# Optimization experiments

Measured on AMD Instinct MI355X. Metric: run time of the kernel, lower is better.

## Reference

```python
import jax, jax.numpy as jnp
import numpy as np
import math

B, S, H, E, TOPK, NHEADS = 8, 512, 1024, 8, 2, 8
CAP = int(B * S * 1.5 * TOPK / E)  # 1536


def _linear(x, w, b):
    # torch nn.Linear convention: y = x @ w.T + b, w: [out, in]
    return x @ w.T + b


def _mha(x, in_w, in_b, out_w, out_b, n_heads):
    # torch nn.MultiheadAttention self-attention, eval mode (no dropout)
    Bx, Sx, D = x.shape
    dh = D // n_heads
    qkv = x @ in_w.T + in_b                      # [B,S,3D]
    q, k, v = jnp.split(qkv, 3, axis=-1)
    def heads(t):
        return t.reshape(Bx, Sx, n_heads, dh).transpose(0, 2, 1, 3)  # [B,h,S,dh]
    q, k, v = heads(q), heads(k), heads(v)
    scores = jnp.einsum('bhqd,bhkd->bhqk', q, k) / math.sqrt(dh)
    attn = jax.nn.softmax(scores, axis=-1)
    o = jnp.einsum('bhqk,bhkd->bhqd', attn, v)   # [B,h,S,dh]
    o = o.transpose(0, 2, 1, 3).reshape(Bx, Sx, D)
    return o @ out_w.T + out_b


def setup_inputs() -> dict:
    key = jax.random.key(0)
    ks = jax.random.split(key, 24)
    sc = 0.02
    d = {
        'hidden_states': jax.random.normal(ks[0], (B, S, H), jnp.float32),
        'pos_emb': jax.random.normal(ks[1], (S, H), jnp.float32) * sc,
        'se_w1': jax.random.normal(ks[2], (H // 4, 1), jnp.float32) * sc,
        'se_b1': jnp.zeros((H // 4,), jnp.float32),
        'se_w2': jax.random.normal(ks[3], (H // 4, H // 4), jnp.float32) * sc,
        'se_b2': jnp.zeros((H // 4,), jnp.float32),
        'sexp_w': jax.random.normal(ks[4], (H, H // 4), jnp.float32) * sc,
        'sexp_b': jnp.zeros((H,), jnp.float32),
        'te_w1': jax.random.normal(ks[5], (H, H + 2), jnp.float32) * sc,
        'te_b1': jnp.zeros((H,), jnp.float32),
        'te_w2': jax.random.normal(ks[6], (H, H), jnp.float32) * sc,
        'te_b2': jnp.zeros((H,), jnp.float32),
        'attn_in_w': jax.random.normal(ks[7], (3 * H, H), jnp.float32) * sc,
        'attn_in_b': jnp.zeros((3 * H,), jnp.float32),
        'attn_out_w': jax.random.normal(ks[8], (H, H), jnp.float32) * sc,
        'attn_out_b': jnp.zeros((H,), jnp.float32),
        'tr_w1': jax.random.normal(ks[9], (H, H), jnp.float32) * sc,
        'tr_b1': jnp.zeros((H,), jnp.float32),
        'tr_w2': jax.random.normal(ks[10], (E, H), jnp.float32) * sc,
        'tr_b2': jnp.zeros((E,), jnp.float32),
    }
    return d


def reference(hidden_states, pos_emb, se_w1, se_b1, se_w2, se_b2, sexp_w, sexp_b,
              te_w1, te_b1, te_w2, te_b2, attn_in_w, attn_in_b, attn_out_w, attn_out_b,
              tr_w1, tr_b1, tr_w2, tr_b2):
    b, s, h = hidden_states.shape
    timestamps = jnp.arange(s, dtype=hidden_states.dtype)           # [S]
    seasonality = jnp.sin(timestamps * 2 * jnp.pi / 24)             # [S]
    ts_b = jnp.broadcast_to(timestamps, (b, s))
    se_b = jnp.broadcast_to(seasonality, (b, s))

    position_embeddings = pos_emb[:s][None]                          # [1,S,H]
    seas = jax.nn.relu(_linear(se_b[..., None], se_w1, se_b1))       # [B,S,H/4]
    seas = _linear(seas, se_w2, se_b2)
    seasonal_embeddings = _linear(seas, sexp_w, sexp_b)              # [B,S,H]

    time_features = jnp.stack([ts_b, se_b], axis=-1)                 # [B,S,2]
    combined = jnp.concatenate([hidden_states, time_features], -1)   # [B,S,H+2]
    enc = jax.nn.relu(_linear(combined, te_w1, te_b1))
    enc = _linear(enc, te_w2, te_b2)
    enc = enc + position_embeddings + seasonal_embeddings
    enc = _mha(enc, attn_in_w, attn_in_b, attn_out_w, attn_out_b, NHEADS)

    logits = _linear(jax.nn.relu(_linear(enc, tr_w1, tr_b1)), tr_w2, tr_b2)  # [B,S,E]
    router_probs = jax.nn.softmax(logits, axis=-1)
    top_k_probs, top_k_idx = jax.lax.top_k(router_probs, TOPK)
    top_k_probs = top_k_probs / top_k_probs.sum(-1, keepdims=True)

    capacity = int(b * s * 1.5 * TOPK / E)
    # top-k indices are distinct per token, so summed one-hots replicate the
    # python loop's slot-0 writes exactly.
    onehot = jax.nn.one_hot(top_k_idx, E, dtype=router_probs.dtype)  # [B,S,K,E]
    disp0 = onehot.sum(axis=2)                                        # [B,S,E]
    comb0 = jnp.einsum('bske,bsk->bse', onehot, top_k_probs)          # [B,S,E]
    dispatch = jnp.zeros((b, s, E, capacity), router_probs.dtype).at[:, :, :, 0].set(disp0)
    combine = jnp.zeros((b, s, E, capacity), router_probs.dtype).at[:, :, :, 0].set(comb0)

    p_mean = router_probs.mean(axis=(0, 1))
    aux_loss = jnp.sum(p_mean * jnp.log(p_mean * E + 1e-9))
    return dispatch, combine, router_probs, aux_loss
```

## Files before the change

kernel.cpp:

```cpp
#include <hip/hip_runtime.h>
#include <hip/hip_bf16.h>


#define Hh 1024

typedef __attribute__((ext_vector_type(8))) short short8v;
typedef __attribute__((ext_vector_type(4))) float f32x4;

static __device__ __forceinline__ ushort f2bf(float x) {
  uint u = __float_as_uint(x);
  u += 0x7FFF + ((u >> 16) & 1);
  return (ushort)(u >> 16);
}
static __device__ __forceinline__ float bf2f(ushort h) {
  return __uint_as_float(((uint)h) << 16);
}

#define KBARRIER() do { \
    __builtin_amdgcn_sched_barrier(0); \
    asm volatile("s_waitcnt lgkmcnt(0)" ::: "memory"); \
    __builtin_amdgcn_sched_barrier(0); \
    __builtin_amdgcn_s_barrier(); \
    __builtin_amdgcn_sched_barrier(0); \
  } while (0)

template<int EPI, bool RELU, bool HAS_BN, bool HAS_BSN>
__global__ __launch_bounds__(256, 2) void mgemm_k(
    const ushort* __restrict__ A, int lda, long long sAmaj, long long sAmin, int aHi, int aLo,
    const ushort* __restrict__ Bf, int BNT, int BKC, long long sBmaj, long long sBmin,
    float* __restrict__ Cf, ushort* __restrict__ Ch, int ldc, long long sCmaj, long long sCmin,
    int splitOff,
    ushort* __restrict__ pK, ushort* __restrict__ pV,
    int Kd, int zdiv,
    const float* __restrict__ bN, const float* __restrict__ bSN, int ldbs, int smod,
    float alpha,
    char* __restrict__ zout, long long zbase, long long zlimit)
{
  int gx = gridDim.x, gy = gridDim.y;
  int lin = (blockIdx.z * gy + blockIdx.y) * gx + blockIdx.x;
  int nwg = gx * gy * gridDim.z;
  int cpx = nwg >> 3;
  int swz = (lin & 7) * cpx + (lin >> 3);
  int bz = swz / (gx * gy);
  int rem = swz - bz * (gx * gy);
  int by = rem / gx, bx = rem - by * gx;

  int zj = bz / zdiv, zi = bz - zj * zdiv;
  A += (size_t)zj * sAmaj + (size_t)zi * sAmin;
  const ushort* bfb = Bf + (size_t)zj * sBmaj + (size_t)zi * sBmin;
  long long coff = (long long)zj * sCmaj + (long long)zi * sCmin;

  int m0 = by * 64, n0 = bx * 128;

  __shared__ __align__(16) ushort smem[16384];

  int t = threadIdx.x;
  int l = t & 63, w = t >> 6;
  int wm = w >> 1, wn = w & 1;

  f32x4 acc[2][4];
#pragma unroll
  for (int i = 0; i < 2; ++i)
#pragma unroll
    for (int j = 0; j < 4; ++j) acc[i][j] = (f32x4){0.f, 0.f, 0.f, 0.f};

  int srow = t >> 2;
  int sc = t & 3;
  const ushort* gAh = A + (size_t)(m0 + srow) * lda + aHi + sc * 8;
  const ushort* gAl = A + (size_t)(m0 + srow) * lda + aLo + sc * 8;
  int wo = (srow * 64 + sc * 16) ^ (((srow >> 1) & 7) << 4);

  int aoff[2];
#pragma unroll
  for (int mi = 0; mi < 2; ++mi) {
    int row = wm * 32 + mi * 16 + (l & 15);
    aoff[mi] = (row * 64 + (l >> 4) * 16) ^ (((row >> 1) & 7) << 4);
  }

  const ushort* bph[4];
  const ushort* bpl[4];
  int ntg0 = (n0 >> 4) + wn * 4;
#pragma unroll
  for (int ni = 0; ni < 4; ++ni) {
    bph[ni] = bfb + ((size_t)(ntg0 + ni) * BKC) * 512 + l * 8;
    bpl[ni] = bfb + ((size_t)(BNT + ntg0 + ni) * BKC) * 512 + l * 8;
  }

  int4 a0h, a0l, a1h, a1l;
  short8v B0h[4], B0l[4], B1h[4], B1l[4];

#define LOADA0(s) { a0h = *(const int4*)(gAh + (s)*32); a0l = *(const int4*)(gAl + (s)*32); }
#define LOADA1(s) { a1h = *(const int4*)(gAh + (s)*32); a1l = *(const int4*)(gAl + (s)*32); }
#define STOREA(h, lo2, base) { char* nb = (char*)smem + (base); \
    *(int4*)(nb + wo) = h; *(int4*)(nb + 4096 + wo) = lo2; }
#define LOADB(BH, BL, s) { _Pragma("unroll") \
    for (int ni = 0; ni < 4; ++ni) { \
      BH[ni] = *(const short8v*)(bph[ni] + (size_t)(s) * 512); \
      BL[ni] = *(const short8v*)(bpl[ni] + (size_t)(s) * 512); } }
#define MFMA_STEP(ahb, alb, BH, BL) { \
    short8v ah[2], al[2]; \
    _Pragma("unroll") for (int mi = 0; mi < 2; ++mi) \
      ah[mi] = *(const short8v*)((char*)smem + (ahb) + aoff[mi]); \
    _Pragma("unroll") for (int mi = 0; mi < 2; ++mi) \
      al[mi] = *(const short8v*)((char*)smem + (alb) + aoff[mi]); \
    _Pragma("unroll") for (int ni = 0; ni < 4; ++ni) \
      _Pragma("unroll") for (int mi = 0; mi < 2; ++mi) \
        acc[mi][ni] = __builtin_amdgcn_mfma_f32_16x16x32_bf16(ah[mi], BH[ni], acc[mi][ni], 0, 0, 0); \
    _Pragma("unroll") for (int ni = 0; ni < 4; ++ni) \
      _Pragma("unroll") for (int mi = 0; mi < 2; ++mi) \
        acc[mi][ni] = __builtin_amdgcn_mfma_f32_16x16x32_bf16(al[mi], BH[ni], acc[mi][ni], 0, 0, 0); \
    _Pragma("unroll") for (int ni = 0; ni < 4; ++ni) \
      _Pragma("unroll") for (int mi = 0; mi < 2; ++mi) \
        acc[mi][ni] = __builtin_amdgcn_mfma_f32_16x16x32_bf16(ah[mi], BL[ni], acc[mi][ni], 0, 0, 0); }

  int nt = Kd >> 5;
  LOADA0(0); LOADB(B0h, B0l, 0);
  LOADA1(1); LOADB(B1h, B1l, 1);
  STOREA(a0h, a0l, 0);
  KBARRIER();
  for (int s2 = 0; s2 < nt; s2 += 2) {
    if (s2 + 2 < nt) LOADA0(s2 + 2);
    MFMA_STEP(0, 4096, B0h, B0l);
    if (s2 + 2 < nt) LOADB(B0h, B0l, s2 + 2);
    STOREA(a1h, a1l, 8192);
    KBARRIER();
    if (s2 + 3 < nt) LOADA1(s2 + 3);
    MFMA_STEP(8192, 12288, B1h, B1l);
    if (s2 + 3 < nt) LOADB(B1h, B1l, s2 + 3);
    if (s2 + 2 < nt) STOREA(a0h, a0l, 0);
    KBARRIER();
  }
#undef LOADA0
#undef LOADA1
#undef STOREA
#undef LOADB
#undef MFMA_STEP

#pragma unroll
  for (int mi = 0; mi < 2; ++mi)
#pragma unroll
    for (int j = 0; j < 4; ++j) {
      int m = m0 + wm * 32 + mi * 16 + (l >> 4) * 4 + j;
#pragma unroll
      for (int ni = 0; ni < 4; ++ni) {
        int n = n0 + wn * 64 + ni * 16 + (l & 15);
        float x = acc[mi][ni][j] * alpha;
        if (HAS_BN) x += bN[n];
        if (HAS_BSN) x += bSN[(size_t)(m % smod) * ldbs + n];
        if (RELU) x = fmaxf(x, 0.f);
        acc[mi][ni][j] = x;
      }
    }

  if (EPI == 0) {
    float* Fs = (float*)smem;
#pragma unroll
    for (int mi = 0; mi < 2; ++mi)
#pragma unroll
      for (int j = 0; j < 4; ++j) {
        int r = wm * 32 + mi * 16 + (l >> 4) * 4 + j;
#pragma unroll
        for (int ni = 0; ni < 4; ++ni) {
          int c = wn * 64 + ni * 16 + (l & 15);
          *(float*)((char*)Fs + ((r * 512 + c * 4) ^ ((r & 7) << 4))) = acc[mi][ni][j];
        }
      }
    __syncthreads();
#pragma unroll
    for (int r8 = 0; r8 < 8; ++r8) {
      int idx = r8 * 256 + t;
      int row = idx >> 5, slot = idx & 31;
      int4 v = *(const int4*)((char*)Fs + ((row * 512 + slot * 16) ^ ((row & 7) << 4)));
      *(int4*)(Cf + coff + (size_t)(m0 + row) * ldc + n0 + slot * 4) = v;
    }
  } else {
    ushort* Es = smem;
    bool isQ = (EPI == 1) || (n0 < 1024);
    bool isK = (EPI == 2) && !isQ && (n0 < 2048);
    int bb = m0 >> 9, s0 = m0 & 511;
    int hh2 = isK ? ((n0 - 1024) >> 7) : ((n0 - 2048) >> 7);
    size_t kvb = (size_t)(bb * 8 + hh2) * 131072;
#pragma unroll
    for (int pass = 0; pass < 2; ++pass) {
      if (!(EPI == 2 && !isQ && !isK)) {
#pragma unroll
        for (int mi = 0; mi < 2; ++mi)
#pragma unroll
          for (int j = 0; j < 4; ++j) {
            int lr = wm * 32 + mi * 16 + (l >> 4) * 4 + j;
#pragma unroll
            for (int ni = 0; ni < 4; ++ni) {
              int lcb = (wn * 64 + ni * 16 + (l & 15)) * 2;
              float x = acc[mi][ni][j];
              ushort h = f2bf(x);
              ushort vv = (pass == 0) ? h : f2bf(x - bf2f(h));
              *(ushort*)((char*)Es + ((lr * 256 + lcb) ^ ((lr & 7) << 4))) = vv;
            }
          }
      } else {
#pragma unroll
        for (int mi = 0; mi < 2; ++mi)
#pragma unroll
          for (int j = 0; j < 4; ++j) {
            int cc = (wm * 32 + mi * 16 + (l >> 4) * 4 + j) * 2;
#pragma unroll
            for (int ni = 0; ni < 4; ++ni) {
              int rr = wn * 64 + ni * 16 + (l & 15);
              float x = acc[mi][ni][j];
              ushort h = f2bf(x);
              ushort vv = (pass == 0) ? h : f2bf(x - bf2f(h));
              *(ushort*)((char*)Es + ((rr * 128 + cc) ^ ((rr & 7) << 4))) = vv;
            }
          }
      }
      __syncthreads();
      if (isQ) {
        int off = (pass == 0) ? 0 : splitOff;
#pragma unroll
        for (int r = 0; r < 4; ++r) {
          int idx = r * 256 + t;
          int row = idx >> 4, cb = (idx & 15) * 16;
          int4 v = *(const int4*)((char*)Es + ((row * 256 + cb) ^ ((row & 7) << 4)));
          *(int4*)((char*)(Ch + coff + (size_t)(m0 + row) * ldc + off + n0) + cb) = v;
        }
      } else if (isK) {
#pragma unroll
        for (int sw = 0; sw < 4; ++sw) {
          int idx = sw * 256 + t;
          int f = idx >> 6, l2 = idx & 63;
          int st = f >> 2, dc = f & 3;
          int row = st * 16 + (l2 & 15);
          int colB = (dc * 32 + ((l2 >> 4) << 3)) * 2;
          short8v v = *(const short8v*)((char*)Es + ((row * 256 + colB) ^ ((row & 7) << 4)));
          *(short8v*)(pK + kvb + (size_t)((pass * 32 + (s0 >> 4) + st) * 4 + dc) * 512 + l2 * 8) = v;
        }
      } else {
#pragma unroll
        for (int sw = 0; sw < 4; ++sw) {
          int idx = sw * 256 + t;
          int f = idx >> 6, l2 = idx & 63;
          int dt = f >> 1, sch = f & 1;
          int row = dt * 16 + (l2 & 15);
          int colB = (sch * 32 + ((l2 >> 4) << 3)) * 2;
          short8v v = *(const short8v*)((char*)Es + ((row * 128 + colB) ^ ((row & 7) << 4)));
          *(short8v*)(pV + kvb + (size_t)((pass * 8 + dt) * 16 + (s0 >> 5) + sch) * 512 + l2 * 8) = v;
        }
      }
      if (pass == 0) __syncthreads();
    }
  }

  if (zlimit > 0) {
    long long zo = zbase + (long long)lin * 65536LL;
    if (zo < zlimit) {
      long long n16 = (zlimit - zo) >> 4;
      if (n16 > 4096) n16 = 4096;
      float4* zp = (float4*)(zout + zo);
      float4 zz = make_float4(0.f, 0.f, 0.f, 0.f);
      for (long long i = t; i < n16; i += 256) zp[i] = zz;
    }
  }
}

__global__ __launch_bounds__(64) void convertf_k(
    const float* __restrict__ W, int ldw, ushort* __restrict__ Wf, int NT, int KC)
{
  int kc = blockIdx.x, nt2 = blockIdx.y, l = threadIdx.x;
  const float* src = W + (size_t)(nt2 * 16 + (l & 15)) * ldw + kc * 32 + ((l >> 4) << 3);
  ushort h8[8], l8[8];
#pragma unroll
  for (int j = 0; j < 8; ++j) {
    float x = src[j];
    h8[j] = f2bf(x);
    l8[j] = f2bf(x - bf2f(h8[j]));
  }
  *(int4*)(Wf + ((size_t)nt2 * KC + kc) * 512 + l * 8) = *(int4*)h8;
  *(int4*)(Wf + ((size_t)(NT + nt2) * KC + kc) * 512 + l * 8) = *(int4*)l8;
}

__global__ __launch_bounds__(256) void convert_k(
    const float* __restrict__ W, int lda, ushort* __restrict__ Whl, int K)
{
  int r = blockIdx.x;
  int c = threadIdx.x * 4;
  const float* src = W + (size_t)r * lda + c;
  float x0 = src[0], x1 = src[1], x2 = src[2], x3 = src[3];
  ushort4 h, lo;
  h.x = f2bf(x0); lo.x = f2bf(x0 - bf2f(h.x));
  h.y = f2bf(x1); lo.y = f2bf(x1 - bf2f(h.y));
  h.z = f2bf(x2); lo.z = f2bf(x2 - bf2f(h.z));
  h.w = f2bf(x3); lo.w = f2bf(x3 - bf2f(h.w));
  ushort* dst = Whl + (size_t)r * 2 * K;
  *(ushort4*)&dst[c] = h;
  *(ushort4*)&dst[K + c] = lo;
}

__global__ __launch_bounds__(256) void precompute_k(
    const float* __restrict__ pos_emb,
    const float* __restrict__ se_w1, const float* __restrict__ se_b1,
    const float* __restrict__ se_w2, const float* __restrict__ se_b2,
    const float* __restrict__ sexp_w, const float* __restrict__ sexp_b,
    const float* __restrict__ te_w1, const float* __restrict__ te_b1,
    float* __restrict__ psea, float* __restrict__ bias1)
{
  int s = blockIdx.x, t = threadIdx.x;
  float ts = (float)s;
  float se = sinf(((ts * 2.0f) * 3.14159274101257324f) / 24.0f);
  __shared__ float l1[256], l2[256];
  l1[t] = fmaxf(se * se_w1[t] + se_b1[t], 0.f);
  __syncthreads();
  {
    float a = se_b2[t];
    const float* wr = se_w2 + (size_t)t * 256;
    for (int i = 0; i < 256; ++i) a += l1[i] * wr[i];
    l2[t] = a;
  }
  __syncthreads();
#pragma unroll
  for (int r = 0; r < 4; ++r) {
    int h = r * 256 + t;
    float v = sexp_b[h];
    const float* wr = sexp_w + (size_t)h * 256;
    for (int j = 0; j < 256; ++j) v += l2[j] * wr[j];
    psea[s * Hh + h] = pos_emb[s * Hh + h] + v;
    bias1[s * Hh + h] = te_b1[h] + ts * te_w1[(size_t)h * 1026 + 1024]
                                 + se * te_w1[(size_t)h * 1026 + 1025];
  }
}

__global__ __launch_bounds__(256) void softmax2_k(ushort* __restrict__ S)
{
  int row = blockIdx.x * 4 + (threadIdx.x >> 6);
  int lane = threadIdx.x & 63;
  ushort* u = S + (size_t)row * 1024;
  int4 hv = *(const int4*)&u[lane * 8];
  int4 lv = *(const int4*)&u[512 + lane * 8];
  ushort h8[8], l8[8];
  *(int4*)h8 = hv; *(int4*)l8 = lv;
  float x[8];
#pragma unroll
  for (int j = 0; j < 8; ++j) x[j] = bf2f(h8[j]) + bf2f(l8[j]);
  float m = x[0];
#pragma unroll
  for (int j = 1; j < 8; ++j) m = fmaxf(m, x[j]);
#pragma unroll
  for (int off = 32; off; off >>= 1) m = fmaxf(m, __shfl_xor(m, off));
  float s = 0.f;
#pragma unroll
  for (int j = 0; j < 8; ++j) { x[j] = expf(x[j] - m); s += x[j]; }
#pragma unroll
  for (int off = 32; off; off >>= 1) s += __shfl_xor(s, off);
  float inv = 1.f / s;
#pragma unroll
  for (int j = 0; j < 8; ++j) {
    float p = x[j] * inv;
    h8[j] = f2bf(p);
    l8[j] = f2bf(p - bf2f(h8[j]));
  }
  *(int4*)&u[lane * 8] = *(int4*)h8;
  *(int4*)&u[512 + lane * 8] = *(int4*)l8;
}

__global__ __launch_bounds__(256) void tr2_k(
    const float* __restrict__ h1, const float* __restrict__ w,
    const float* __restrict__ bias, float* __restrict__ logits)
{
  int wid = threadIdx.x >> 6, lane = threadIdx.x & 63;
  int t = blockIdx.x * 4 + wid;
  const float* x = h1 + (size_t)t * Hh;
  float acc[8];
#pragma unroll
  for (int e = 0; e < 8; ++e) acc[e] = 0.f;
  for (int k = lane; k < Hh; k += 64) {
    float xv = x[k];
#pragma unroll
    for (int e = 0; e < 8; ++e) acc[e] += xv * w[e * Hh + k];
  }
#pragma unroll
  for (int e = 0; e < 8; ++e) {
#pragma unroll
    for (int off = 32; off; off >>= 1) acc[e] += __shfl_xor(acc[e], off);
  }
  if (lane == 0) {
#pragma unroll
    for (int e = 0; e < 8; ++e) logits[(size_t)t * 8 + e] = acc[e] + bias[e];
  }
}

__global__ __launch_bounds__(256) void fill0_k(float4* __restrict__ p, long long n4)
{
  long long i = (long long)blockIdx.x * 256 + threadIdx.x;
  long long stride = (long long)gridDim.x * 256;
  float4 z = make_float4(0.f, 0.f, 0.f, 0.f);
  for (; i < n4; i += stride) p[i] = z;
}

__global__ __launch_bounds__(256) void router_k(
    float* __restrict__ out, float* __restrict__ partials)
{
  int t = blockIdx.x * 256 + threadIdx.x;
  float* lg = out + 100663296 + (size_t)t * 8;
  float p[8];
#pragma unroll
  for (int e = 0; e < 8; ++e) p[e] = lg[e];
  float m = p[0];
#pragma unroll
  for (int e = 1; e < 8; ++e) m = fmaxf(m, p[e]);
  float s = 0.f;
#pragma unroll
  for (int e = 0; e < 8; ++e) { p[e] = expf(p[e] - m); s += p[e]; }
  float inv = 1.f / s;
#pragma unroll
  for (int e = 0; e < 8; ++e) p[e] *= inv;
#pragma unroll
  for (int e = 0; e < 8; ++e) lg[e] = p[e];

  int i0 = 0; float v0 = p[0];
#pragma unroll
  for (int e = 1; e < 8; ++e) if (p[e] > v0) { v0 = p[e]; i0 = e; }
  int i1 = -1; float v1 = -1.f;
#pragma unroll
  for (int e = 0; e < 8; ++e) if (e != i0 && p[e] > v1) { v1 = p[e]; i1 = e; }
  float wn = 1.f / (v0 + v1);
  size_t db = (size_t)t * (8 * 1536);
  out[db + (size_t)i0 * 1536] = 1.f;
  out[db + (size_t)i1 * 1536] = 1.f;
  out[50331648 + db + (size_t)i0 * 1536] = v0 * wn;
  out[50331648 + db + (size_t)i1 * 1536] = v1 * wn;

  __shared__ float red[256];
#pragma unroll
  for (int e = 0; e < 8; ++e) {
    red[threadIdx.x] = p[e];
    __syncthreads();
    for (int st = 128; st; st >>= 1) {
      if (threadIdx.x < st) red[threadIdx.x] += red[threadIdx.x + st];
      __syncthreads();
    }
    if (threadIdx.x == 0) partials[blockIdx.x * 8 + e] = red[0];
    __syncthreads();
  }
}

__global__ __launch_bounds__(64) void aux_k(float* __restrict__ partials,
                                            float* __restrict__ out)
{
  int lane = threadIdx.x;
  float v = 0.f;
  if (lane < 8) {
    float s = 0.f;
    for (int b = 0; b < 16; ++b) s += partials[b * 8 + lane];
    float pm = s / 4096.f;
    v = pm * logf(pm * 8.f + 1e-9f);
  }
#pragma unroll
  for (int off = 4; off; off >>= 1) v += __shfl_xor(v, off);
  if (lane == 0) out[100696064] = v;
  partials[lane] = 0.f;
  partials[64 + lane] = 0.f;
}

extern "C" void kernel_launch(void* const* d_in, const int* in_sizes, int n_in,
                              void* d_out, int out_size, void* d_ws, size_t ws_size,
                              hipStream_t stream)
{
  const float* hidden = (const float*)d_in[0];
  const float* pos_emb = (const float*)d_in[1];
  const float* se_w1 = (const float*)d_in[2];
  const float* se_b1 = (const float*)d_in[3];
  const float* se_w2 = (const float*)d_in[4];
  const float* se_b2 = (const float*)d_in[5];
  const float* sexp_w = (const float*)d_in[6];
  const float* sexp_b = (const float*)d_in[7];
  const float* te_w1 = (const float*)d_in[8];
  const float* te_b1 = (const float*)d_in[9];
  const float* te_w2 = (const float*)d_in[10];
  const float* te_b2 = (const float*)d_in[11];
  const float* ain_w = (const float*)d_in[12];
  const float* ain_b = (const float*)d_in[13];
  const float* aout_w = (const float*)d_in[14];
  const float* aout_b = (const float*)d_in[15];
  const float* tr_w1 = (const float*)d_in[16];
  const float* tr_b1 = (const float*)d_in[17];
  const float* tr_w2 = (const float*)d_in[18];
  const float* tr_b2 = (const float*)d_in[19];
  float* out = (float*)d_out;
  char* ob = (char*)d_out;

  const long long COMB = 201326592LL;
  ushort* W1f  = (ushort*)(ob + COMB + 0);
  ushort* W2f  = (ushort*)(ob + COMB + 4194304);
  ushort* Waf  = (ushort*)(ob + COMB + 8388608);
  ushort* Wof  = (ushort*)(ob + COMB + 20971520);
  ushort* Wtf  = (ushort*)(ob + COMB + 25165824);
  float*  psea = (float*)(ob + COMB + 29360128);
  float*  bias1= (float*)(ob + COMB + 31457280);
  ushort* hid2 = (ushort*)(ob + COMB + 33554432);
  float*  h1   = (float*)(ob + COMB + 33554432);
  ushort* enc1 = (ushort*)(ob + COMB + 50331648);
  ushort* attno= (ushort*)(ob + COMB + 50331648);
  ushort* enc2 = (ushort*)(ob + COMB + 67108864);
  ushort* encf = (ushort*)(ob + COMB + 67108864);
  ushort* qbuf = (ushort*)(ob + COMB + 83886080);
  ushort* Kf   = (ushort*)(ob + COMB + 100663296);
  ushort* Vf   = (ushort*)(ob + COMB + 117440512);
  ushort* scorS= (ushort*)(ob + COMB + 134217728);
  float*  parts= (float*)(ob + COMB + 167772160);
  float*  lgts = out + 100663296;

  convertf_k<<<dim3(32, 64), 64, 0, stream>>>(te_w1, 1026, W1f, 64, 32);
  convertf_k<<<dim3(32, 64), 64, 0, stream>>>(te_w2, 1024, W2f, 64, 32);
  convertf_k<<<dim3(32, 192), 64, 0, stream>>>(ain_w, 1024, Waf, 192, 32);
  convertf_k<<<dim3(32, 64), 64, 0, stream>>>(aout_w, 1024, Wof, 64, 32);
  convertf_k<<<dim3(32, 64), 64, 0, stream>>>(tr_w1, 1024, Wtf, 64, 32);
  convert_k<<<4096, 256, 0, stream>>>(hidden, 1024, hid2, 1024);

  precompute_k<<<512, 256, 0, stream>>>(pos_emb, se_w1, se_b1, se_w2, se_b2,
                                        sexp_w, sexp_b, te_w1, te_b1, psea, bias1);

  mgemm_k<1, true, false, true><<<dim3(8, 64, 1), 256, 0, stream>>>(
      hid2, 2048, 0, 0, 0, 1024,
      W1f, 64, 32, 0, 0,
      nullptr, enc1, 2048, 0, 0, 1024, nullptr, nullptr,
      1024, 1, nullptr, bias1, 1024, 512, 1.f,
      ob, 0LL, 33554432LL);

  mgemm_k<1, false, true, true><<<dim3(8, 64, 1), 256, 0, stream>>>(
      enc1, 2048, 0, 0, 0, 1024,
      W2f, 64, 32, 0, 0,
      nullptr, enc2, 2048, 0, 0, 1024, nullptr, nullptr,
      1024, 1, te_b2, psea, 1024, 512, 1.f,
      ob, 33554432LL, 67108864LL);

  mgemm_k<2, false, true, false><<<dim3(24, 64, 1), 256, 0, stream>>>(
      enc2, 2048, 0, 0, 0, 1024,
      Waf, 192, 32, 0, 0,
      nullptr, qbuf, 2048, 0, 0, 1024, Kf, Vf,
      1024, 1, ain_b, nullptr, 1, 1, 1.f,
      ob, 67108864LL, 167772160LL);

  mgemm_k<1, false, false, false><<<dim3(4, 8, 64), 256, 0, stream>>>(
      qbuf, 2048, 1048576, 128, 0, 1024,
      Kf, 32, 4, 1048576, 131072,
      nullptr, scorS, 1024, 4194304, 524288, 512, nullptr, nullptr,
      128, 8, nullptr, nullptr, 1, 1, 0.08838834764831845f,
      nullptr, 0LL, 0LL);

  softmax2_k<<<8192, 256, 0, stream>>>(scorS);

  mgemm_k<1, false, false, false><<<dim3(1, 8, 64), 256, 0, stream>>>(
      scorS, 1024, 4194304, 524288, 0, 512,
      Vf, 8, 16, 1048576, 131072,
      nullptr, attno, 2048, 1048576, 128, 1024, nullptr, nullptr,
      512, 8, nullptr, nullptr, 1, 1, 1.f,
      nullptr, 0LL, 0LL);

  mgemm_k<1, false, true, false><<<dim3(8, 64, 1), 256, 0, stream>>>(
      attno, 2048, 0, 0, 0, 1024,
      Wof, 64, 32, 0, 0,
      nullptr, encf, 2048, 0, 0, 1024, nullptr, nullptr,
      1024, 1, aout_b, nullptr, 1, 1, 1.f,
      ob, 167772160LL, 201326592LL);

  mgemm_k<0, true, true, false><<<dim3(8, 64, 1), 256, 0, stream>>>(
      encf, 2048, 0, 0, 0, 1024,
      Wtf, 64, 32, 0, 0,
      h1, nullptr, 1024, 0, 0, 0, nullptr, nullptr,
      1024, 1, tr_b1, nullptr, 1, 1, 1.f,
      nullptr, 0LL, 0LL);

  tr2_k<<<1024, 256, 0, stream>>>(h1, tr_w2, tr_b2, lgts);

  fill0_k<<<2048, 256, 0, stream>>>((float4*)(out + 50331648), 12582912LL);

  router_k<<<16, 256, 0, stream>>>(out, parts);
  aux_k<<<1, 64, 0, stream>>>(parts, out);
}
```

Baseline: 498.8 us.

## Halve GEMM N-tile to 64, raise occupancy, and spread output zeroing across kernels

The GEMM tile shrinks from 64x128 to 64x64 with half the LDS, and launch bounds rise to 4 blocks per SM. Grids double to give more workgroups and better CU fill. The K/V epilogue gains a d-half index so each block writes its part of the packed layout. The workspace is reordered so that zeroing the dispatch/combine region is spread as tails over more kernels, including the attention-V GEMM, trN GEMM and tr2. The five weight conversions merge into one launch. The smaller tile lowers B-operand reuse per A tile load and raises global traffic for A, in exchange for occupancy and fewer launches.

```diff
diff --git a/kernel.cpp b/kernel.cpp
--- a/kernel.cpp
+++ b/kernel.cpp
@@ -24,8 +24,24 @@
     __builtin_amdgcn_sched_barrier(0); \
   } while (0)
 
+static __device__ __forceinline__ void ztail(char* zout, long long zbase,
+                                             long long zlimit, long long zchunk,
+                                             int lin, int t, int bdim) {
+  if (zlimit > 0) {
+    long long zo = zbase + (long long)lin * zchunk;
+    if (zo < zlimit) {
+      long long n16 = (zlimit - zo) >> 4;
+      long long c16 = zchunk >> 4;
+      if (n16 > c16) n16 = c16;
+      float4* zp = (float4*)(zout + zo);
+      float4 zz = make_float4(0.f, 0.f, 0.f, 0.f);
+      for (long long i = t; i < n16; i += bdim) zp[i] = zz;
+    }
+  }
+}
+
 template<int EPI, bool RELU, bool HAS_BN, bool HAS_BSN>
-__global__ __launch_bounds__(256, 2) void mgemm_k(
+__global__ __launch_bounds__(256, 4) void mgemm_k(
     const ushort* __restrict__ A, int lda, long long sAmaj, long long sAmin, int aHi, int aLo,
     const ushort* __restrict__ Bf, int BNT, int BKC, long long sBmaj, long long sBmin,
     float* __restrict__ Cf, ushort* __restrict__ Ch, int ldc, long long sCmaj, long long sCmin,
@@ -34,7 +50,7 @@
     int Kd, int zdiv,
     const float* __restrict__ bN, const float* __restrict__ bSN, int ldbs, int smod,
     float alpha,
-    char* __restrict__ zout, long long zbase, long long zlimit)
+    char* __restrict__ zout, long long zbase, long long zlimit, long long zchunk)
 {
   int gx = gridDim.x, gy = gridDim.y;
   int lin = (blockIdx.z * gy + blockIdx.y) * gx + blockIdx.x;
@@ -50,19 +66,19 @@
   const ushort* bfb = Bf + (size_t)zj * sBmaj + (size_t)zi * sBmin;
   long long coff = (long long)zj * sCmaj + (long long)zi * sCmin;
 
-  int m0 = by * 64, n0 = bx * 128;
-
-  __shared__ __align__(16) ushort smem[16384];
+  int m0 = by * 64, n0 = bx * 64;
+
+  __shared__ __align__(16) ushort smem[8192];
 
   int t = threadIdx.x;
   int l = t & 63, w = t >> 6;
   int wm = w >> 1, wn = w & 1;
 
-  f32x4 acc[2][4];
+  f32x4 acc[2][2];
 #pragma unroll
   for (int i = 0; i < 2; ++i)
 #pragma unroll
-    for (int j = 0; j < 4; ++j) acc[i][j] = (f32x4){0.f, 0.f, 0.f, 0.f};
+    for (int j = 0; j < 2; ++j) acc[i][j] = (f32x4){0.f, 0.f, 0.f, 0.f};
 
   int srow = t >> 2;
   int sc = t & 3;
@@ -77,24 +93,24 @@
     aoff[mi] = (row * 64 + (l >> 4) * 16) ^ (((row >> 1) & 7) << 4);
   }
 
-  const ushort* bph[4];
-  const ushort* bpl[4];
-  int ntg0 = (n0 >> 4) + wn * 4;
-#pragma unroll
-  for (int ni = 0; ni < 4; ++ni) {
+  const ushort* bph[2];
+  const ushort* bpl[2];
+  int ntg0 = (n0 >> 4) + wn * 2;
+#pragma unroll
+  for (int ni = 0; ni < 2; ++ni) {
     bph[ni] = bfb + ((size_t)(ntg0 + ni) * BKC) * 512 + l * 8;
     bpl[ni] = bfb + ((size_t)(BNT + ntg0 + ni) * BKC) * 512 + l * 8;
   }
 
   int4 a0h, a0l, a1h, a1l;
-  short8v B0h[4], B0l[4], B1h[4], B1l[4];
+  short8v B0h[2], B0l[2], B1h[2], B1l[2];
 
 #define LOADA0(s) { a0h = *(const int4*)(gAh + (s)*32); a0l = *(const int4*)(gAl + (s)*32); }
 #define LOADA1(s) { a1h = *(const int4*)(gAh + (s)*32); a1l = *(const int4*)(gAl + (s)*32); }
 #define STOREA(h, lo2, base) { char* nb = (char*)smem + (base); \
     *(int4*)(nb + wo) = h; *(int4*)(nb + 4096 + wo) = lo2; }
 #define LOADB(BH, BL, s) { _Pragma("unroll") \
-    for (int ni = 0; ni < 4; ++ni) { \
+    for (int ni = 0; ni < 2; ++ni) { \
       BH[ni] = *(const short8v*)(bph[ni] + (size_t)(s) * 512); \
       BL[ni] = *(const short8v*)(bpl[ni] + (size_t)(s) * 512); } }
 #define MFMA_STEP(ahb, alb, BH, BL) { \
@@ -103,13 +119,13 @@
       ah[mi] = *(const short8v*)((char*)smem + (ahb) + aoff[mi]); \
     _Pragma("unroll") for (int mi = 0; mi < 2; ++mi) \
       al[mi] = *(const short8v*)((char*)smem + (alb) + aoff[mi]); \
-    _Pragma("unroll") for (int ni = 0; ni < 4; ++ni) \
+    _Pragma("unroll") for (int ni = 0; ni < 2; ++ni) \
       _Pragma("unroll") for (int mi = 0; mi < 2; ++mi) \
         acc[mi][ni] = __builtin_amdgcn_mfma_f32_16x16x32_bf16(ah[mi], BH[ni], acc[mi][ni], 0, 0, 0); \
-    _Pragma("unroll") for (int ni = 0; ni < 4; ++ni) \
+    _Pragma("unroll") for (int ni = 0; ni < 2; ++ni) \
       _Pragma("unroll") for (int mi = 0; mi < 2; ++mi) \
         acc[mi][ni] = __builtin_amdgcn_mfma_f32_16x16x32_bf16(al[mi], BH[ni], acc[mi][ni], 0, 0, 0); \
-    _Pragma("unroll") for (int ni = 0; ni < 4; ++ni) \
+    _Pragma("unroll") for (int ni = 0; ni < 2; ++ni) \
       _Pragma("unroll") for (int mi = 0; mi < 2; ++mi) \
         acc[mi][ni] = __builtin_amdgcn_mfma_f32_16x16x32_bf16(ah[mi], BL[ni], acc[mi][ni], 0, 0, 0); }
 
@@ -142,8 +158,8 @@
     for (int j = 0; j < 4; ++j) {
       int m = m0 + wm * 32 + mi * 16 + (l >> 4) * 4 + j;
 #pragma unroll
-      for (int ni = 0; ni < 4; ++ni) {
-        int n = n0 + wn * 64 + ni * 16 + (l & 15);
+      for (int ni = 0; ni < 2; ++ni) {
+        int n = n0 + wn * 32 + ni * 16 + (l & 15);
         float x = acc[mi][ni][j] * alpha;
         if (HAS_BN) x += bN[n];
         if (HAS_BSN) x += bSN[(size_t)(m % smod) * ldbs + n];
@@ -152,6 +168,8 @@
       }
     }
 
+  __syncthreads();
+
   if (EPI == 0) {
     float* Fs = (float*)smem;
 #pragma unroll
@@ -160,17 +178,17 @@
       for (int j = 0; j < 4; ++j) {
         int r = wm * 32 + mi * 16 + (l >> 4) * 4 + j;
 #pragma unroll
-        for (int ni = 0; ni < 4; ++ni) {
-          int c = wn * 64 + ni * 16 + (l & 15);
-          *(float*)((char*)Fs + ((r * 512 + c * 4) ^ ((r & 7) << 4))) = acc[mi][ni][j];
+        for (int ni = 0; ni < 2; ++ni) {
+          int c = wn * 32 + ni * 16 + (l & 15);
+          *(float*)((char*)Fs + ((r * 256 + c * 4) ^ ((r & 7) << 4))) = acc[mi][ni][j];
         }
       }
     __syncthreads();
 #pragma unroll
-    for (int r8 = 0; r8 < 8; ++r8) {
-      int idx = r8 * 256 + t;
-      int row = idx >> 5, slot = idx & 31;
-      int4 v = *(const int4*)((char*)Fs + ((row * 512 + slot * 16) ^ ((row & 7) << 4)));
+    for (int r4 = 0; r4 < 4; ++r4) {
+      int idx = r4 * 256 + t;
+      int row = idx >> 4, slot = idx & 15;
+      int4 v = *(const int4*)((char*)Fs + ((row * 256 + slot * 16) ^ ((row & 7) << 4)));
       *(int4*)(Cf + coff + (size_t)(m0 + row) * ldc + n0 + slot * 4) = v;
     }
   } else {
@@ -179,6 +197,7 @@
     bool isK = (EPI == 2) && !isQ && (n0 < 2048);
     int bb = m0 >> 9, s0 = m0 & 511;
     int hh2 = isK ? ((n0 - 1024) >> 7) : ((n0 - 2048) >> 7);
+    int dhalf = isK ? (((n0 - 1024) >> 6) & 1) : (((n0 - 2048) >> 6) & 1);
     size_t kvb = (size_t)(bb * 8 + hh2) * 131072;
 #pragma unroll
     for (int pass = 0; pass < 2; ++pass) {
@@ -189,12 +208,12 @@
           for (int j = 0; j < 4; ++j) {
             int lr = wm * 32 + mi * 16 + (l >> 4) * 4 + j;
 #pragma unroll
-            for (int ni = 0; ni < 4; ++ni) {
-              int lcb = (wn * 64 + ni * 16 + (l & 15)) * 2;
+            for (int ni = 0; ni < 2; ++ni) {
+              int lcb = (wn * 32 + ni * 16 + (l & 15)) * 2;
               float x = acc[mi][ni][j];
               ushort h = f2bf(x);
               ushort vv = (pass == 0) ? h : f2bf(x - bf2f(h));
-              *(ushort*)((char*)Es + ((lr * 256 + lcb) ^ ((lr & 7) << 4))) = vv;
+              *(ushort*)((char*)Es + ((lr * 128 + lcb) ^ ((lr & 7) << 4))) = vv;
             }
           }
       } else {
@@ -204,8 +223,8 @@
           for (int j = 0; j < 4; ++j) {
             int cc = (wm * 32 + mi * 16 + (l >> 4) * 4 + j) * 2;
 #pragma unroll
-            for (int ni = 0; ni < 4; ++ni) {
-              int rr = wn * 64 + ni * 16 + (l & 15);
+            for (int ni = 0; ni < 2; ++ni) {
+              int rr = wn * 32 + ni * 16 + (l & 15);
               float x = acc[mi][ni][j];
               ushort h = f2bf(x);
               ushort vv = (pass == 0) ? h : f2bf(x - bf2f(h));
@@ -215,57 +234,59 @@
       }
       __syncthreads();
       if (isQ) {
-        int off = (pass == 0) ? 0 : splitOff;
-#pragma unroll
-        for (int r = 0; r < 4; ++r) {
+#pragma unroll
+        for (int r = 0; r < 2; ++r) {
           int idx = r * 256 + t;
-          int row = idx >> 4, cb = (idx & 15) * 16;
-          int4 v = *(const int4*)((char*)Es + ((row * 256 + cb) ^ ((row & 7) << 4)));
+          int row = idx >> 3, cb = (idx & 7) * 16;
+          int off = (pass == 0) ? 0 : splitOff;
+          int4 v = *(const int4*)((char*)Es + ((row * 128 + cb) ^ ((row & 7) << 4)));
           *(int4*)((char*)(Ch + coff + (size_t)(m0 + row) * ldc + off + n0) + cb) = v;
         }
       } else if (isK) {
 #pragma unroll
-        for (int sw = 0; sw < 4; ++sw) {
+        for (int sw = 0; sw < 2; ++sw) {
           int idx = sw * 256 + t;
           int f = idx >> 6, l2 = idx & 63;
-          int st = f >> 2, dc = f & 3;
+          int st = f >> 1, dc = f & 1;
           int row = st * 16 + (l2 & 15);
-          int colB = (dc * 32 + ((l2 >> 4) << 3)) * 2;
-          short8v v = *(const short8v*)((char*)Es + ((row * 256 + colB) ^ ((row & 7) << 4)));
-          *(short8v*)(pK + kvb + (size_t)((pass * 32 + (s0 >> 4) + st) * 4 + dc) * 512 + l2 * 8) = v;
+          int colB = dc * 64 + ((l2 >> 4) << 4);
+          short8v v = *(const short8v*)((char*)Es + ((row * 128 + colB) ^ ((row & 7) << 4)));
+          int kc = dhalf * 2 + dc;
+          *(short8v*)(pK + kvb + (size_t)((pass * 32 + (s0 >> 4) + st) * 4 + kc) * 512 + l2 * 8) = v;
         }
       } else {
 #pragma unroll
-        for (int sw = 0; sw < 4; ++sw) {
+        for (int sw = 0; sw < 2; ++sw) {
           int idx = sw * 256 + t;
           int f = idx >> 6, l2 = idx & 63;
-          int dt = f >> 1, sch = f & 1;
-          int row = dt * 16 + (l2 & 15);
-          int colB = (sch * 32 + ((l2 >> 4) << 3)) * 2;
+          int ntL = f >> 1, sc2 = f & 1;
+          int row = ntL * 16 + (l2 & 15);
+          int colB = sc2 * 64 + ((l2 >> 4) << 4);
           short8v v = *(const short8v*)((char*)Es + ((row * 128 + colB) ^ ((row & 7) << 4)));
-          *(short8v*)(pV + kvb + (size_t)((pass * 8 + dt) * 16 + (s0 >> 5) + sch) * 512 + l2 * 8) = v;
+          int ntd = dhalf * 4 + ntL;
+          int kc = (s0 >> 5) + sc2;
+          *(short8v*)(pV + kvb + (size_t)((pass * 8 + ntd) * 16 + kc) * 512 + l2 * 8) = v;
         }
       }
       if (pass == 0) __syncthreads();
     }
   }
 
-  if (zlimit > 0) {
-    long long zo = zbase + (long long)lin * 65536LL;
-    if (zo < zlimit) {
-      long long n16 = (zlimit - zo) >> 4;
-      if (n16 > 4096) n16 = 4096;
-      float4* zp = (float4*)(zout + zo);
-      float4 zz = make_float4(0.f, 0.f, 0.f, 0.f);
-      for (long long i = t; i < n16; i += 256) zp[i] = zz;
-    }
-  }
-}
-
-__global__ __launch_bounds__(64) void convertf_k(
-    const float* __restrict__ W, int ldw, ushort* __restrict__ Wf, int NT, int KC)
-{
-  int kc = blockIdx.x, nt2 = blockIdx.y, l = threadIdx.x;
+  ztail(zout, zbase, zlimit, zchunk, lin, t, 256);
+}
+
+__global__ __launch_bounds__(64) void convall_k(
+    const float* __restrict__ te_w1, const float* __restrict__ te_w2,
+    const float* __restrict__ ain_w, const float* __restrict__ aout_w,
+    const float* __restrict__ tr_w1, ushort* __restrict__ base)
+{
+  int kc = blockIdx.x, y = blockIdx.y, l = threadIdx.x;
+  const float* W; int ldw, NT, nt2; ushort* dst;
+  if (y < 64)       { W = te_w1;  ldw = 1026; NT = 64;  nt2 = y;       dst = base; }
+  else if (y < 128) { W = te_w2;  ldw = 1024; NT = 64;  nt2 = y - 64;  dst = base + 2097152; }
+  else if (y < 320) { W = ain_w;  ldw = 1024; NT = 192; nt2 = y - 128; dst = base + 4194304; }
+  else if (y < 384) { W = aout_w; ldw = 1024; NT = 64;  nt2 = y - 320; dst = base + 10485760; }
+  else              { W = tr_w1;  ldw = 1024; NT = 64;  nt2 = y - 384; dst = base + 12582912; }
   const float* src = W + (size_t)(nt2 * 16 + (l & 15)) * ldw + kc * 32 + ((l >> 4) << 3);
   ushort h8[8], l8[8];
 #pragma unroll
@@ -274,8 +295,8 @@
     h8[j] = f2bf(x);
     l8[j] = f2bf(x - bf2f(h8[j]));
   }
-  *(int4*)(Wf + ((size_t)nt2 * KC + kc) * 512 + l * 8) = *(int4*)h8;
-  *(int4*)(Wf + ((size_t)(NT + nt2) * KC + kc) * 512 + l * 8) = *(int4*)l8;
+  *(int4*)(dst + ((size_t)nt2 * 32 + kc) * 512 + l * 8) = *(int4*)h8;
+  *(int4*)(dst + ((size_t)(NT + nt2) * 32 + kc) * 512 + l * 8) = *(int4*)l8;
 }
 
 __global__ __launch_bounds__(256) void convert_k(
@@ -363,7 +384,8 @@
 
 __global__ __launch_bounds__(256) void tr2_k(
     const float* __restrict__ h1, const float* __restrict__ w,
-    const float* __restrict__ bias, float* __restrict__ logits)
+    const float* __restrict__ bias, float* __restrict__ logits,
+    char* __restrict__ zout, long long zbase, long long zlimit, long long zchunk)
 {
   int wid = threadIdx.x >> 6, lane = threadIdx.x & 63;
   int t = blockIdx.x * 4 + wid;
@@ -385,6 +407,7 @@
 #pragma unroll
     for (int e = 0; e < 8; ++e) logits[(size_t)t * 8 + e] = acc[e] + bias[e];
   }
+  ztail(zout, zbase, zlimit, zchunk, blockIdx.x, threadIdx.x, 256);
 }
 
 __global__ __launch_bounds__(256) void fill0_k(float4* __restrict__ p, long long n4)
@@ -488,90 +511,82 @@
   char* ob = (char*)d_out;
 
   const long long COMB = 201326592LL;
-  ushort* W1f  = (ushort*)(ob + COMB + 0);
-  ushort* W2f  = (ushort*)(ob + COMB + 4194304);
-  ushort* Waf  = (ushort*)(ob + COMB + 8388608);
-  ushort* Wof  = (ushort*)(ob + COMB + 20971520);
-  ushort* Wtf  = (ushort*)(ob + COMB + 25165824);
+  ushort* Wbase = (ushort*)(ob + COMB);
   float*  psea = (float*)(ob + COMB + 29360128);
   float*  bias1= (float*)(ob + COMB + 31457280);
-  ushort* hid2 = (ushort*)(ob + COMB + 33554432);
-  float*  h1   = (float*)(ob + COMB + 33554432);
-  ushort* enc1 = (ushort*)(ob + COMB + 50331648);
-  ushort* attno= (ushort*)(ob + COMB + 50331648);
-  ushort* enc2 = (ushort*)(ob + COMB + 67108864);
-  ushort* encf = (ushort*)(ob + COMB + 67108864);
-  ushort* qbuf = (ushort*)(ob + COMB + 83886080);
-  ushort* Kf   = (ushort*)(ob + COMB + 100663296);
-  ushort* Vf   = (ushort*)(ob + COMB + 117440512);
-  ushort* scorS= (ushort*)(ob + COMB + 134217728);
+  ushort* attno= (ushort*)(ob + COMB + 33554432);
+  ushort* enc1 = (ushort*)(ob + COMB + 33554432);
+  ushort* encf = (ushort*)(ob + COMB + 50331648);
+  ushort* enc2 = (ushort*)(ob + COMB + 50331648);
+  ushort* qbuf = (ushort*)(ob + COMB + 67108864);
+  ushort* Kf   = (ushort*)(ob + COMB + 83886080);
+  ushort* Vf   = (ushort*)(ob + COMB + 100663296);
+  ushort* scorS= (ushort*)(ob + COMB + 117440512);
+  ushort* hid2 = (ushort*)(ob + COMB + 150994944);
+  float*  h1   = (float*)(ob + COMB + 150994944);
   float*  parts= (float*)(ob + COMB + 167772160);
   float*  lgts = out + 100663296;
 
-  convertf_k<<<dim3(32, 64), 64, 0, stream>>>(te_w1, 1026, W1f, 64, 32);
-  convertf_k<<<dim3(32, 64), 64, 0, stream>>>(te_w2, 1024, W2f, 64, 32);
-  convertf_k<<<dim3(32, 192), 64, 0, stream>>>(ain_w, 1024, Waf, 192, 32);
-  convertf_k<<<dim3(32, 64), 64, 0, stream>>>(aout_w, 1024, Wof, 64, 32);
-  convertf_k<<<dim3(32, 64), 64, 0, stream>>>(tr_w1, 1024, Wtf, 64, 32);
+  convall_k<<<dim3(32, 448), 64, 0, stream>>>(te_w1, te_w2, ain_w, aout_w, tr_w1, Wbase);
   convert_k<<<4096, 256, 0, stream>>>(hidden, 1024, hid2, 1024);
-
   precompute_k<<<512, 256, 0, stream>>>(pos_emb, se_w1, se_b1, se_w2, se_b2,
                                         sexp_w, sexp_b, te_w1, te_b1, psea, bias1);
 
-  mgemm_k<1, true, false, true><<<dim3(8, 64, 1), 256, 0, stream>>>(
+  mgemm_k<1, true, false, true><<<dim3(16, 64, 1), 256, 0, stream>>>(
       hid2, 2048, 0, 0, 0, 1024,
-      W1f, 64, 32, 0, 0,
+      Wbase, 64, 32, 0, 0,
       nullptr, enc1, 2048, 0, 0, 1024, nullptr, nullptr,
       1024, 1, nullptr, bias1, 1024, 512, 1.f,
-      ob, 0LL, 33554432LL);
-
-  mgemm_k<1, false, true, true><<<dim3(8, 64, 1), 256, 0, stream>>>(
+      ob, 0LL, 33554432LL, 32768LL);
+
+  mgemm_k<1, false, true, true><<<dim3(16, 64, 1), 256, 0, stream>>>(
       enc1, 2048, 0, 0, 0, 1024,
-      W2f, 64, 32, 0, 0,
+      Wbase + 2097152, 64, 32, 0, 0,
       nullptr, enc2, 2048, 0, 0, 1024, nullptr, nullptr,
       1024, 1, te_b2, psea, 1024, 512, 1.f,
-      ob, 33554432LL, 67108864LL);
-
-  mgemm_k<2, false, true, false><<<dim3(24, 64, 1), 256, 0, stream>>>(
+      ob, 33554432LL, 67108864LL, 32768LL);
+
+  mgemm_k<2, false, true, false><<<dim3(48, 64, 1), 256, 0, stream>>>(
       enc2, 2048, 0, 0, 0, 1024,
-      Waf, 192, 32, 0, 0,
+      Wbase + 4194304, 192, 32, 0, 0,
       nullptr, qbuf, 2048, 0, 0, 1024, Kf, Vf,
       1024, 1, ain_b, nullptr, 1, 1, 1.f,
-      ob, 67108864LL, 167772160LL);
-
-  mgemm_k<1, false, false, false><<<dim3(4, 8, 64), 256, 0, stream>>>(
+      ob, 67108864LL, 167772160LL, 32768LL);
+
+  mgemm_k<1, false, false, false><<<dim3(8, 8, 64), 256, 0, stream>>>(
       qbuf, 2048, 1048576, 128, 0, 1024,
       Kf, 32, 4, 1048576, 131072,
       nullptr, scorS, 1024, 4194304, 524288, 512, nullptr, nullptr,
       128, 8, nullptr, nullptr, 1, 1, 0.08838834764831845f,
-      nullptr, 0LL, 0LL);
+      nullptr, 0LL, 0LL, 0LL);
 
   softmax2_k<<<8192, 256, 0, stream>>>(scorS);
 
-  mgemm_k<1, false, false, false><<<dim3(1, 8, 64), 256, 0, stream>>>(
+  mgemm_k<1, false, false, false><<<dim3(2, 8, 64), 256, 0, stream>>>(
       scorS, 1024, 4194304, 524288, 0, 512,
       Vf, 8, 16, 1048576, 131072,
       nullptr, attno, 2048, 1048576, 128, 1024, nullptr, nullptr,
       512, 8, nullptr, nullptr, 1, 1, 1.f,
-      nullptr, 0LL, 0LL);
-
-  mgemm_k<1, false, true, false><<<dim3(8, 64, 1), 256, 0, stream>>>(
+      ob, COMB + 67108864LL, COMB + 100663296LL, 32768LL);
+
+  mgemm_k<1, false, true, false><<<dim3(16, 64, 1), 256, 0, stream>>>(
       attno, 2048, 0, 0, 0, 1024,
-      Wof, 64, 32, 0, 0,
+      Wbase + 10485760, 64, 32, 0, 0,
       nullptr, encf, 2048, 0, 0, 1024, nullptr, nullptr,
       1024, 1, aout_b, nullptr, 1, 1, 1.f,
-      ob, 167772160LL, 201326592LL);
-
-  mgemm_k<0, true, true, false><<<dim3(8, 64, 1), 256, 0, stream>>>(
+      ob, 167772160LL, 201326592LL, 32768LL);
+
+  mgemm_k<0, true, true, false><<<dim3(16, 64, 1), 256, 0, stream>>>(
       encf, 2048, 0, 0, 0, 1024,
-      Wtf, 64, 32, 0, 0,
+      Wbase + 12582912, 64, 32, 0, 0,
       h1, nullptr, 1024, 0, 0, 0, nullptr, nullptr,
       1024, 1, tr_b1, nullptr, 1, 1, 1.f,
-      nullptr, 0LL, 0LL);
-
-  tr2_k<<<1024, 256, 0, stream>>>(h1, tr_w2, tr_b2, lgts);
-
-  fill0_k<<<2048, 256, 0, stream>>>((float4*)(out + 50331648), 12582912LL);
+      ob, COMB + 100663296LL, COMB + 150994944LL, 49152LL);
+
+  tr2_k<<<1024, 256, 0, stream>>>(h1, tr_w2, tr_b2, lgts,
+                                  ob, COMB + 0LL, COMB + 67108864LL, 65536LL);
+
+  fill0_k<<<2048, 256, 0, stream>>>((float4*)(ob + COMB + 150994944), 3145728LL);
 
   router_k<<<16, 256, 0, stream>>>(out, parts);
   aux_k<<<1, 64, 0, stream>>>(parts, out);
```

New measurement: 529.2 us. +6.1%, slower.
